# Kernel optimization log

Measured on AMD Instinct MI355X. Metric: run time of the kernel, lower is better.

The kernel has to match this reference:

```python
import jax, jax.numpy as jnp
import numpy as np

N_QUBITS = 4
DIM = 2 ** N_QUBITS  # 16
CLASS_NUM = 10
BATCH = 2_097_152

# bit tables (constants): LBITS little-endian (prob2amp path, sample 0),
# HBITS big-endian (resolve path, samples 1..B-1)
_k = np.arange(DIM)
LBITS = jnp.asarray(((_k[:, None] >> np.arange(N_QUBITS)[None, :]) & 1).astype(np.float32))
HBITS = jnp.asarray(((_k[:, None] >> (N_QUBITS - 1 - np.arange(N_QUBITS))[None, :]) & 1).astype(np.float32))

_I2 = jnp.eye(2, dtype=jnp.float32)
_SWAP = jnp.array([[1, 0, 0, 0], [0, 0, 1, 0], [0, 1, 0, 0], [0, 0, 0, 1]], dtype=jnp.float32)
_CZ = jnp.diag(jnp.array([1.0, 1.0, 1.0, -1.0], dtype=jnp.float32))


def _ry(t):
    c, s = jnp.cos(t / 2), jnp.sin(t / 2)
    return jnp.stack([jnp.stack([c, -s]), jnp.stack([s, c])])


def _ry_layer(thetas):  # kron(ry(th[n-1]), ..., ry(th[0])) as in qf_ry
    M = jnp.ones((1, 1), dtype=jnp.float32)
    for i in range(N_QUBITS):
        M = jnp.kron(_ry(thetas[i]), M)
    return M


def _swap_mat(index):  # qf_swap_dec matrix
    M = jnp.ones((1, 1), dtype=jnp.float32)
    for _ in range(index - 1):
        M = jnp.kron(_I2, M)
    M = jnp.kron(_SWAP, M)
    for _ in range(N_QUBITS - 1 - index):
        M = jnp.kron(_I2, M)
    return M


def _cz_core(i1):
    M = jnp.ones((1, 1), dtype=jnp.float32)
    for _ in range(i1):
        M = jnp.kron(_I2, M)
    M = jnp.kron(_CZ, M)
    for _ in range(N_QUBITS - 2 - i1):
        M = jnp.kron(_I2, M)
    return M


def _cz_mat(i1, i2):  # qf_cz as a matrix (incl. swap conjugation)
    M = jnp.eye(DIM, dtype=jnp.float32)
    for i in range(i2, i1 + 1, -1):
        M = _swap_mat(i) @ M
    M = _cz_core(i1) @ M
    for i in range(i1 + 2, i2 + 1):
        M = _swap_mat(i) @ M
    return M


def _build_unitary(theta):  # vqc_10 as one 16x16 matrix
    U = _ry_layer(theta[:N_QUBITS])
    for i in range(N_QUBITS - 1):  # CZ(2,3), CZ(1,2), CZ(0,1)
        U = _cz_mat(N_QUBITS - 2 - i, N_QUBITS - 1 - i) @ U
    U = _cz_mat(0, N_QUBITS - 1) @ U  # CZ(0,3) via swaps
    U = _ry_layer(theta[N_QUBITS:]) @ U
    return U


def setup_inputs() -> dict:
    key = jax.random.key(0)
    kx, _ = jax.random.split(key)
    x = jax.random.uniform(kx, (BATCH, N_QUBITS), dtype=jnp.float32)
    theta = jnp.array([np.pi / 3, np.pi / 4, np.pi / 3, np.pi / 9,
                       np.pi, np.pi / 4, np.pi / 10, np.pi / 2], dtype=jnp.float32)
    return {"x": x, "theta": theta}


def reference(x, theta):
    U = _build_unitary(theta)
    # sample 0: prob2amp (little-endian, raw products, no sqrt)
    x0 = x[0]  # [4]
    amp0 = jnp.ones((DIM,), dtype=x.dtype)
    for j in range(N_QUBITS):
        amp0 = amp0 * jnp.where(LBITS[:, j] == 1, x0[j], 1 - x0[j])
    # samples 1..B-1: resolve (square probs, big-endian bits, sqrt)
    p2 = x[1:] ** 2  # [B-1,4]
    acc = jnp.ones((x.shape[0] - 1, DIM), dtype=x.dtype)
    for j in range(N_QUBITS):
        acc = acc * jnp.where(HBITS[None, :, j] == 1, p2[:, j:j + 1], 1 - p2[:, j:j + 1])
    ampR = jnp.sqrt(acc)
    amps = jnp.concatenate([amp0[None, :], ampR], axis=0)  # [B,16]
    probs = (amps @ U.T) ** 2  # state_prob after circuit
    return probs[:, :CLASS_NUM]
```

## Files before the change

kernel.cpp:

```cpp
#include <hip/hip_runtime.h>
#include <hip/hip_bf16.h>


typedef float f32x4 __attribute__((ext_vector_type(4)));

#if defined(__has_builtin)
#if __has_builtin(__builtin_amdgcn_sqrtf)
#define FSQRT(x) __builtin_amdgcn_sqrtf(x)
#endif
#endif
#ifndef FSQRT
#define FSQRT(x) sqrtf(x)
#endif

__device__ __forceinline__ float ry_el(float c, float s, int i, int j) {
    return (i == j) ? c : (i ? s : -s);
}

__global__ void build_T(const float* __restrict__ theta, float* __restrict__ T) {
    int t = threadIdx.x;
    if (t >= 160) return;
    int c = t >> 4;
    int j = t & 15;

    float co1[4], si1[4], co2[4], si2[4];
#pragma unroll
    for (int q = 0; q < 4; ++q) {
        float h1 = 0.5f * theta[q];
        float h2 = 0.5f * theta[4 + q];
        co1[q] = cosf(h1); si1[q] = sinf(h1);
        co2[q] = cosf(h2); si2[q] = sinf(h2);
    }
    float acc = 0.0f;
#pragma unroll
    for (int k = 0; k < 16; ++k) {
        int k0 = k & 1, k1 = (k >> 1) & 1, k2 = (k >> 2) & 1, k3 = (k >> 3) & 1;
        float r2 = ry_el(co2[0], si2[0], c & 1, k0)
                 * ry_el(co2[1], si2[1], (c >> 1) & 1, k1)
                 * ry_el(co2[2], si2[2], (c >> 2) & 1, k2)
                 * ry_el(co2[3], si2[3], (c >> 3) & 1, k3);
        float r1 = ry_el(co1[0], si1[0], k0, j & 1)
                 * ry_el(co1[1], si1[1], k1, (j >> 1) & 1)
                 * ry_el(co1[2], si1[2], k2, (j >> 2) & 1)
                 * ry_el(co1[3], si1[3], k3, (j >> 3) & 1);
        int sgn = (k0 & k1) ^ (k1 & k2) ^ (k2 & k3) ^ (k0 & k3);
        acc = fmaf(sgn ? -r2 : r2, r1, acc);
    }
    T[c * 16 + j] = acc;
}

__device__ __forceinline__ void amp_resolve(f32x4 xv, float amp[16]) {
    float p0 = xv.x * xv.x, p1 = xv.y * xv.y;
    float p2 = xv.z * xv.z, p3 = xv.w * xv.w;
    float hi[4] = { (1.0f - p0) * (1.0f - p1), (1.0f - p0) * p1,
                    p0 * (1.0f - p1),          p0 * p1 };
    float lo[4] = { (1.0f - p2) * (1.0f - p3), (1.0f - p2) * p3,
                    p2 * (1.0f - p3),          p2 * p3 };
    float sh[4], sl[4];
#pragma unroll
    for (int i = 0; i < 4; ++i) { sh[i] = FSQRT(hi[i]); sl[i] = FSQRT(lo[i]); }
#pragma unroll
    for (int k = 0; k < 16; ++k)
        amp[k] = sh[k >> 2] * sl[k & 3];
}

__device__ __forceinline__ void amp_prob2amp(f32x4 xv, float amp[16]) {
    float lo[4] = { (1.0f - xv.x) * (1.0f - xv.y), xv.x * (1.0f - xv.y),
                    (1.0f - xv.x) * xv.y,          xv.x * xv.y };
    float hi[4] = { (1.0f - xv.z) * (1.0f - xv.w), xv.z * (1.0f - xv.w),
                    (1.0f - xv.z) * xv.w,          xv.z * xv.w };
#pragma unroll
    for (int k = 0; k < 16; ++k)
        amp[k] = lo[k & 3] * hi[k >> 2];
}

#define TILES 4

__global__ __launch_bounds__(256, 8) void vqc_main(const f32x4* __restrict__ x,
                                                   const float* __restrict__ T,
                                                   float* __restrict__ out,
                                                   int nsamp) {
    __shared__ float sBuf[4][2][640];

    int tid = threadIdx.x;
    int wid = tid >> 6;
    int lane = tid & 63;

    long long base = (long long)blockIdx.x * (TILES * 256);

    f32x4 xv[TILES];
#pragma unroll
    for (int t = 0; t < TILES; ++t) {
        long long bt = base + (long long)t * 256 + tid;
        if (bt < nsamp) xv[t] = x[bt];
    }

#pragma unroll
    for (int t = 0; t < TILES; ++t) {
        long long tileStart = base + (long long)t * 256;
        long long b = tileStart + tid;

        int p = t & 1;
        float* myBuf = sBuf[wid][p];

        if (b < nsamp) {
            float amp[16];
            if (b == 0) amp_prob2amp(xv[t], amp);
            else        amp_resolve(xv[t], amp);

#pragma unroll 2
            for (int c = 0; c < 10; ++c) {
                float s = 0.0f;
#pragma unroll
                for (int jj = 0; jj < 16; ++jj)
                    s = fmaf(T[c * 16 + jj], amp[jj], s);
                myBuf[lane * 10 + c] = s * s;
            }
        }

        asm volatile("s_waitcnt lgkmcnt(0)" ::: "memory");

        long long waveBase = tileStart + (long long)(wid << 6);
        long long wrem = (long long)nsamp - waveBase;
        if (wrem >= 64) {
            f32x4* ov = (f32x4*)(out + waveBase * 10);
            const f32x4* sv = (const f32x4*)myBuf;
#pragma unroll
            for (int i = lane; i < 160; i += 64)
                __builtin_nontemporal_store(sv[i], &ov[i]);
        } else if (wrem > 0) {
            int n = (int)wrem * 10;
            for (int i = lane; i < n; i += 64)
                out[waveBase * 10 + i] = myBuf[i];
        }
    }
}

extern "C" void kernel_launch(void* const* d_in, const int* in_sizes, int n_in,
                              void* d_out, int out_size, void* d_ws, size_t ws_size,
                              hipStream_t stream) {
    const float* x = (const float*)d_in[0];
    const float* theta = (const float*)d_in[1];
    float* out = (float*)d_out;
    float* T = (float*)d_ws;

    int nsamp = in_sizes[0] / 4;

    build_T<<<1, 192, 0, stream>>>(theta, T);

    int spb = TILES * 256;
    int blocks = (nsamp + spb - 1) / spb;
    vqc_main<<<blocks, 256, 0, stream>>>((const f32x4*)x, T, out, nsamp);
}
```

Before: 27.68 us.

## Replace precomputed 16x16 unitary matvec with in-kernel RY butterflies and CZ signs

```diff
diff --git a/kernel.cpp b/kernel.cpp
--- a/kernel.cpp
+++ b/kernel.cpp
@@ -1,5 +1,4 @@
 #include <hip/hip_runtime.h>
-#include <hip/hip_bf16.h>
 
 
 typedef float f32x4 __attribute__((ext_vector_type(4)));
@@ -12,42 +11,6 @@
 #ifndef FSQRT
 #define FSQRT(x) sqrtf(x)
 #endif
-
-__device__ __forceinline__ float ry_el(float c, float s, int i, int j) {
-    return (i == j) ? c : (i ? s : -s);
-}
-
-__global__ void build_T(const float* __restrict__ theta, float* __restrict__ T) {
-    int t = threadIdx.x;
-    if (t >= 160) return;
-    int c = t >> 4;
-    int j = t & 15;
-
-    float co1[4], si1[4], co2[4], si2[4];
-#pragma unroll
-    for (int q = 0; q < 4; ++q) {
-        float h1 = 0.5f * theta[q];
-        float h2 = 0.5f * theta[4 + q];
-        co1[q] = cosf(h1); si1[q] = sinf(h1);
-        co2[q] = cosf(h2); si2[q] = sinf(h2);
-    }
-    float acc = 0.0f;
-#pragma unroll
-    for (int k = 0; k < 16; ++k) {
-        int k0 = k & 1, k1 = (k >> 1) & 1, k2 = (k >> 2) & 1, k3 = (k >> 3) & 1;
-        float r2 = ry_el(co2[0], si2[0], c & 1, k0)
-                 * ry_el(co2[1], si2[1], (c >> 1) & 1, k1)
-                 * ry_el(co2[2], si2[2], (c >> 2) & 1, k2)
-                 * ry_el(co2[3], si2[3], (c >> 3) & 1, k3);
-        float r1 = ry_el(co1[0], si1[0], k0, j & 1)
-                 * ry_el(co1[1], si1[1], k1, (j >> 1) & 1)
-                 * ry_el(co1[2], si1[2], k2, (j >> 2) & 1)
-                 * ry_el(co1[3], si1[3], k3, (j >> 3) & 1);
-        int sgn = (k0 & k1) ^ (k1 & k2) ^ (k2 & k3) ^ (k0 & k3);
-        acc = fmaf(sgn ? -r2 : r2, r1, acc);
-    }
-    T[c * 16 + j] = acc;
-}
 
 __device__ __forceinline__ void amp_resolve(f32x4 xv, float amp[16]) {
     float p0 = xv.x * xv.x, p1 = xv.y * xv.y;
@@ -77,7 +40,7 @@
 #define TILES 4
 
 __global__ __launch_bounds__(256, 8) void vqc_main(const f32x4* __restrict__ x,
-                                                   const float* __restrict__ T,
+                                                   const float* __restrict__ theta,
                                                    float* __restrict__ out,
                                                    int nsamp) {
     __shared__ float sBuf[4][2][640];
@@ -95,6 +58,15 @@
         if (bt < nsamp) xv[t] = x[bt];
     }
 
+    float c1[4], s1[4], c2[4], s2[4];
+#pragma unroll
+    for (int q = 0; q < 4; ++q) {
+        float h1 = 0.5f * theta[q];
+        float h2 = 0.5f * theta[4 + q];
+        c1[q] = __cosf(h1); s1[q] = __sinf(h1);
+        c2[q] = __cosf(h2); s2[q] = __sinf(h2);
+    }
+
 #pragma unroll
     for (int t = 0; t < TILES; ++t) {
         long long tileStart = base + (long long)t * 256;
@@ -108,14 +80,41 @@
             if (b == 0) amp_prob2amp(xv[t], amp);
             else        amp_resolve(xv[t], amp);
 
-#pragma unroll 2
-            for (int c = 0; c < 10; ++c) {
-                float s = 0.0f;
+#define BFLY(Q, CC, SS)                                                  \
+            _Pragma("unroll")                                            \
+            for (int i0 = 0; i0 < 16; ++i0)                              \
+                if (!(i0 & (1 << (Q)))) {                                \
+                    int i1 = i0 | (1 << (Q));                            \
+                    float a0 = amp[i0], a1 = amp[i1];                    \
+                    amp[i0] = fmaf((CC), a0, -(SS) * a1);                \
+                    amp[i1] = fmaf((SS), a0,  (CC) * a1);                \
+                }
+
+            BFLY(0, c1[0], s1[0])
+            BFLY(1, c1[1], s1[1])
+            BFLY(2, c1[2], s1[2])
+            BFLY(3, c1[3], s1[3])
+
+            amp[3]  = -amp[3];
+            amp[6]  = -amp[6];
+            amp[9]  = -amp[9];
+            amp[12] = -amp[12];
+
+            BFLY(0, c2[0], s2[0])
+            BFLY(1, c2[1], s2[1])
+            BFLY(2, c2[2], s2[2])
+#undef BFLY
+
+            float r[10];
 #pragma unroll
-                for (int jj = 0; jj < 16; ++jj)
-                    s = fmaf(T[c * 16 + jj], amp[jj], s);
-                myBuf[lane * 10 + c] = s * s;
-            }
+            for (int i = 0; i < 8; ++i)
+                r[i] = fmaf(c2[3], amp[i], -s2[3] * amp[i + 8]);
+            r[8] = fmaf(s2[3], amp[0], c2[3] * amp[8]);
+            r[9] = fmaf(s2[3], amp[1], c2[3] * amp[9]);
+
+#pragma unroll
+            for (int c = 0; c < 10; ++c)
+                myBuf[lane * 10 + c] = r[c] * r[c];
         }
 
         asm volatile("s_waitcnt lgkmcnt(0)" ::: "memory");
@@ -142,13 +141,9 @@
     const float* x = (const float*)d_in[0];
     const float* theta = (const float*)d_in[1];
     float* out = (float*)d_out;
-    float* T = (float*)d_ws;
 
     int nsamp = in_sizes[0] / 4;
-
-    build_T<<<1, 192, 0, stream>>>(theta, T);
-
     int spb = TILES * 256;
     int blocks = (nsamp + spb - 1) / spb;
-    vqc_main<<<blocks, 256, 0, stream>>>((const f32x4*)x, T, out, nsamp);
+    vqc_main<<<blocks, 256, 0, stream>>>((const f32x4*)x, theta, out, nsamp);
 }
```

Result: faster. 23.90 us (-13.7%).
